# Optimization experiments

Measured on AMD Instinct MI355X. Metric: run time of the kernel, lower is better.

## Reference

```python
import jax, jax.numpy as jnp
import numpy as np

B, N, K = 4, 32768, 16
IN_DIM, HID, OUT_DIM = 32, 64, 32
N_DIM = 2
KIN = 2 * N_DIM + OUT_DIM  # 36
KH = 64
EPS = 1e-5


def _gelu(x):
    return jax.nn.gelu(x, approximate=False)  # torch F.gelu default (erf)


def setup_inputs() -> dict:
    key = jax.random.key(0)
    ks = jax.random.split(key, 16)
    s = lambda fan_in: 1.0 / np.sqrt(fan_in)
    return {
        "inp": jax.random.normal(ks[0], (B, N, IN_DIM), jnp.float32),
        "input_grid": jax.random.uniform(ks[1], (N, N_DIM), jnp.float32),
        "output_grid": jax.random.uniform(ks[2], (N, N_DIM), jnp.float32),
        "neighbor_idx": jax.random.randint(ks[3], (N, K), 0, N, jnp.int32),
        # pointwise projection MLP: in_dim -> hid -> out_dim, GELU between
        "Wp1": jax.random.normal(ks[4], (IN_DIM, HID), jnp.float32) * s(IN_DIM),
        "bp1": jnp.zeros((HID,), jnp.float32),
        "Wp2": jax.random.normal(ks[5], (HID, OUT_DIM), jnp.float32) * s(HID),
        "bp2": jnp.zeros((OUT_DIM,), jnp.float32),
        # per-edge kernel MLP: [2*n_dim+out_dim, 64, 64, out_dim], GELU between
        "Wk1": jax.random.normal(ks[6], (KIN, KH), jnp.float32) * s(KIN),
        "bk1": jnp.zeros((KH,), jnp.float32),
        "Wk2": jax.random.normal(ks[7], (KH, KH), jnp.float32) * s(KH),
        "bk2": jnp.zeros((KH,), jnp.float32),
        "Wk3": jax.random.normal(ks[8], (KH, OUT_DIM), jnp.float32) * s(KH),
        "bk3": jnp.zeros((OUT_DIM,), jnp.float32),
        # LayerNorm
        "ln_gamma": jnp.ones((OUT_DIM,), jnp.float32),
        "ln_beta": jnp.zeros((OUT_DIM,), jnp.float32),
    }


def reference(inp, input_grid, output_grid, neighbor_idx,
              Wp1, bp1, Wp2, bp2, Wk1, bk1, Wk2, bk2, Wk3, bk3,
              ln_gamma, ln_beta):
    # pointwise projection MLP
    x = _gelu(jnp.einsum('bnc,ch->bnh', inp, Wp1) + bp1)
    x = jnp.einsum('bnh,ho->bno', x, Wp2) + bp2  # (B, N, OUT_DIM)

    # neighbor gather (fixed K neighbors per output point)
    f_y = x[:, neighbor_idx, :]                      # (B, N, K, C)
    y_pos = input_grid[neighbor_idx]                 # (N, K, n_dim)
    x_pos = jnp.broadcast_to(output_grid[:, None, :], (N, K, N_DIM))
    pos_feat = jnp.concatenate([y_pos, x_pos], axis=-1)          # (N, K, 2*n_dim)
    agg = jnp.concatenate(
        [jnp.broadcast_to(pos_feat[None], (x.shape[0], N, K, 2 * N_DIM)), f_y],
        axis=-1)                                      # (B, N, K, KIN)

    # nonlinear kernel MLP k(x, y, f(y))
    h = _gelu(jnp.einsum('bnkc,ch->bnkh', agg, Wk1) + bk1)
    h = _gelu(jnp.einsum('bnkh,hg->bnkg', h, Wk2) + bk2)
    k_out = jnp.einsum('bnkg,go->bnko', h, Wk3) + bk3  # (B, N, K, OUT_DIM)

    # mean-aggregate over neighbors (integral transform)
    out = jnp.mean(k_out, axis=2)                      # (B, N, OUT_DIM)

    # residual (shapes match) + LayerNorm over channels
    out = out + x
    mu = jnp.mean(out, axis=-1, keepdims=True)
    var = jnp.mean((out - mu) ** 2, axis=-1, keepdims=True)
    out = (out - mu) * jax.lax.rsqrt(var + EPS) * ln_gamma + ln_beta
    return out
```

## Files before the change

### kernel.cpp

```cpp
#include <hip/hip_runtime.h>

#define BB 4
#define NN 32768
#define KKN 16
#define IN_DIM 32
#define HID 64
#define OUT_DIM 32
#define KH 64
#define WS 88
#define TOT (BB * NN)
#define NWAVES 4096

typedef _Float16 f16;
typedef f16 f16x2 __attribute__((ext_vector_type(2)));
typedef f16 f16x4 __attribute__((ext_vector_type(4)));
typedef f16 f16x8 __attribute__((ext_vector_type(8)));
typedef float f32x4 __attribute__((ext_vector_type(4)));
typedef __fp16 hf16x2 __attribute__((ext_vector_type(2)));
typedef unsigned int u32x4 __attribute__((ext_vector_type(4)));

#define H2(c) ((f16x2){(f16)(c), (f16)(c)})
#define U2(c) (__builtin_bit_cast(unsigned, H2(c)))

__device__ __forceinline__ unsigned cvt2u(float a, float b) {
    hf16x2 r = __builtin_amdgcn_cvt_pkrtz(a, b);
    return __builtin_bit_cast(unsigned, r);
}
__device__ __forceinline__ f16x2 cvt2(float a, float b) {
    hf16x2 r = __builtin_amdgcn_cvt_pkrtz(a, b);
    return __builtin_bit_cast(f16x2, r);
}

__device__ __forceinline__ unsigned pk_fma(unsigned a, unsigned b, unsigned c) {
    unsigned d;
    asm("v_pk_fma_f16 %0, %1, %2, %3" : "=v"(d) : "v"(a), "v"(b), "v"(c));
    return d;
}
__device__ __forceinline__ unsigned pk_mul(unsigned a, unsigned b) {
    unsigned d;
    asm("v_pk_mul_f16 %0, %1, %2" : "=v"(d) : "v"(a), "v"(b));
    return d;
}
__device__ __forceinline__ unsigned pk_add(unsigned a, unsigned b) {
    unsigned d;
    asm("v_pk_add_f16 %0, %1, %2" : "=v"(d) : "v"(a), "v"(b));
    return d;
}
__device__ __forceinline__ unsigned pk_max(unsigned a, unsigned b) {
    unsigned d;
    asm("v_pk_max_f16 %0, %1, %2" : "=v"(d) : "v"(a), "v"(b));
    return d;
}
__device__ __forceinline__ unsigned pk_min(unsigned a, unsigned b) {
    unsigned d;
    asm("v_pk_min_f16 %0, %1, %2" : "=v"(d) : "v"(a), "v"(b));
    return d;
}

struct GeluK {
    unsigned n35, p35, q4, c5, c4, c3, c2, c1, c0, half;
};
__device__ __forceinline__ GeluK gelu_consts() {
    GeluK k;
    k.n35  = U2(-3.5f);        k.p35 = U2(3.5f);
    k.q4   = U2(0.25f);        k.half = U2(0.5f);
    k.c5   = U2(-1.0110344f);  k.c4 = U2(2.85016064f);
    k.c3   = U2(-3.40439040f); k.c2 = U2(2.32402432f);
    k.c1   = U2(-1.04974080f); k.c0 = U2(0.39879504f);
    return k;
}

__device__ __forceinline__ unsigned gelu2u(unsigned x, const GeluK& k) {
    unsigned s  = pk_min(pk_max(x, k.n35), k.p35);
    unsigned s4 = pk_mul(s, k.q4);
    unsigned t  = pk_mul(s4, s4);
    unsigned g  = pk_fma(k.c5, t, k.c4);
    g = pk_fma(g, t, k.c3);
    g = pk_fma(g, t, k.c2);
    g = pk_fma(g, t, k.c1);
    g = pk_fma(g, t, k.c0);
    unsigned h  = pk_fma(s, g, k.half);
    return pk_mul(x, h);
}
__device__ __forceinline__ unsigned gelu2bu(float a, float b, unsigned bias, const GeluK& k) {
    return gelu2u(pk_add(cvt2u(a, b), bias), k);
}
__device__ __forceinline__ unsigned gelu2nu(float a, float b, const GeluK& k) {
    return gelu2u(cvt2u(a, b), k);
}

template <int CTRL>
__device__ __forceinline__ float dppadd(float v) {
    union { float f; int i; } u, r;
    u.f = v;
    r.i = __builtin_amdgcn_update_dpp(0, u.i, CTRL, 0xf, 0xf, true);
    return v + r.f;
}
__device__ __forceinline__ float rowsum16(float v) {
    v = dppadd<0xB1>(v);
    v = dppadd<0x4E>(v);
    v = dppadd<0x124>(v);
    v = dppadd<0x128>(v);
    return v;
}

__global__ __launch_bounds__(256) void point_mlp_kernel(
    const float* __restrict__ inp, const float* __restrict__ Wp1,
    const float* __restrict__ bp1, const float* __restrict__ Wp2,
    const float* __restrict__ bp2, f16* __restrict__ xhf)
{
    __shared__ __align__(16) f16 hb[4][16 * WS];
    const int tid = threadIdx.x, w = tid >> 6, lane = tid & 63;
    const int q = lane >> 4, nl = lane & 15;
    const GeluK gk = gelu_consts();

    f16x8 w1f[4];
    #pragma unroll
    for (int nb = 0; nb < 4; nb++)
        #pragma unroll
        for (int j = 0; j < 8; j++)
            w1f[nb][j] = (f16)Wp1[(q * 8 + j) * HID + nb * 16 + nl];
    f16x8 w2f[2][2];
    #pragma unroll
    for (int nb = 0; nb < 2; nb++)
        #pragma unroll
        for (int c = 0; c < 2; c++)
            #pragma unroll
            for (int j = 0; j < 8; j++) {
                int k = c * 32 + q * 8 + j, kp = ((k & 3) << 4) | (k >> 2);
                w2f[nb][c][j] = (f16)Wp2[kp * OUT_DIM + nb * 16 + nl];
            }
    const unsigned b1q0 = cvt2u(bp1[nl],      bp1[16 + nl]);
    const unsigned b1q1 = cvt2u(bp1[32 + nl], bp1[48 + nl]);
    float b2v[2];
    b2v[0] = bp2[nl]; b2v[1] = bp2[16 + nl];
    const f32x4 zq = (f32x4){0.f, 0.f, 0.f, 0.f};

    const int gw = blockIdx.x * 4 + w;
    const int nw = gridDim.x * 4;

    for (int t = gw; t < TOT / 16; t += nw) {
        const int R = t * 16;
        const float* ap = inp + (size_t)(R + nl) * IN_DIM + q * 8;
        float4 av0 = *(const float4*)ap, av1 = *(const float4*)(ap + 4);
        f16x2 p01 = cvt2(av0.x, av0.y);
        f16x2 p23 = cvt2(av0.z, av0.w);
        f16x2 p45 = cvt2(av1.x, av1.y);
        f16x2 p67 = cvt2(av1.z, av1.w);
        f16x8 af = (f16x8){p01.x, p01.y, p23.x, p23.y, p45.x, p45.y, p67.x, p67.y};

        f32x4 acc[4];
        #pragma unroll
        for (int nb = 0; nb < 4; nb++)
            acc[nb] = __builtin_amdgcn_mfma_f32_16x16x32_f16(af, w1f[nb], zq, 0, 0, 0);

        #pragma unroll
        for (int r = 0; r < 4; r++) {
            unsigned h01 = gelu2bu(acc[0][r], acc[1][r], b1q0, gk);
            unsigned h23 = gelu2bu(acc[2][r], acc[3][r], b1q1, gk);
            *(uint2*)&hb[w][(q * 4 + r) * WS + nl * 4] = (uint2){h01, h23};
        }
        f16x8 a0 = *(const f16x8*)&hb[w][nl * WS + q * 8];
        f16x8 a1 = *(const f16x8*)&hb[w][nl * WS + 32 + q * 8];
        f32x4 a2[2];
        #pragma unroll
        for (int nb = 0; nb < 2; nb++) {
            a2[nb] = (f32x4){b2v[nb], b2v[nb], b2v[nb], b2v[nb]};
            a2[nb] = __builtin_amdgcn_mfma_f32_16x16x32_f16(a0, w2f[nb][0], a2[nb], 0, 0, 0);
            a2[nb] = __builtin_amdgcn_mfma_f32_16x16x32_f16(a1, w2f[nb][1], a2[nb], 0, 0, 0);
        }
        #pragma unroll
        for (int r = 0; r < 4; r++)
            #pragma unroll
            for (int nb = 0; nb < 2; nb++)
                xhf[(size_t)(R + q * 4 + r) * OUT_DIM + nb * 16 + nl] = (f16)a2[nb][r];
    }
}

__global__ __launch_bounds__(256) void gnn_edge_kernel(
    const f16*   __restrict__ xhf,
    const float* __restrict__ igrid, const float* __restrict__ ogrid,
    const int*   __restrict__ nbi,
    const float* __restrict__ Wk1, const float* __restrict__ bk1,
    const float* __restrict__ Wk2, const float* __restrict__ bk2,
    const float* __restrict__ Wk3, const float* __restrict__ bk3,
    const float* __restrict__ gma, const float* __restrict__ bta,
    float* __restrict__ out)
{
    __shared__ __align__(16) f16 tile[8][16 * WS];

    const int tid = threadIdx.x, w = tid >> 6, lane = tid & 63;
    const int q = lane >> 4, nl = lane & 15;
    f16* __restrict__ TA = tile[w * 2];
    f16* __restrict__ TB = tile[w * 2 + 1];
    const GeluK gk = gelu_consts();

    f16x8 w1f[4][2], w2f[4][2], w3f[2][2];
    #pragma unroll
    for (int nb = 0; nb < 4; nb++) {
        #pragma unroll
        for (int j = 0; j < 8; j++) {
            w1f[nb][0][j] = (f16)Wk1[(4 + q * 8 + j) * KH + nb * 16 + nl];
            float v1 = 0.0f;
            if (j < 4 && q == 0) v1 = Wk1[j * KH + nb * 16 + nl];
            w1f[nb][1][j] = (f16)v1;
        }
        #pragma unroll
        for (int c = 0; c < 2; c++)
            #pragma unroll
            for (int j = 0; j < 8; j++) {
                int k = c * 32 + q * 8 + j, kp = ((k & 3) << 4) | (k >> 2);
                w2f[nb][c][j] = (f16)Wk2[kp * KH + nb * 16 + nl];
            }
    }
    #pragma unroll
    for (int nb = 0; nb < 2; nb++)
        #pragma unroll
        for (int c = 0; c < 2; c++)
            #pragma unroll
            for (int j = 0; j < 8; j++) {
                int k = c * 32 + q * 8 + j, kp = ((k & 3) << 4) | (k >> 2);
                w3f[nb][c][j] = (f16)(Wk3[kp * OUT_DIM + nb * 16 + nl] * 0.0625f);
            }

    const unsigned b1q0 = cvt2u(bk1[nl],      bk1[16 + nl]);
    const unsigned b1q1 = cvt2u(bk1[32 + nl], bk1[48 + nl]);
    const unsigned b2q0 = cvt2u(bk2[nl],      bk2[16 + nl]);
    const unsigned b2q1 = cvt2u(bk2[32 + nl], bk2[48 + nl]);
    float b3v[2];
    b3v[0] = bk3[nl]; b3v[1] = bk3[16 + nl];
    const float g0 = gma[nl], g1 = gma[16 + nl], be0 = bta[nl], be1 = bta[16 + nl];

    const f32x4 zq = (f32x4){0.f, 0.f, 0.f, 0.f};

    const int gw = blockIdx.x * 4 + w;

    int tA = gw, tB = gw + NWAVES;
    int nA = nbi[(tA & (NN - 1)) * KKN + nl];
    int nB = nbi[(tB & (NN - 1)) * KKN + nl];
    uint4 fyA = ((const uint4*)(xhf + ((size_t)((tA >> 15) * NN + nA)) * OUT_DIM))[q];
    uint4 fyB = ((const uint4*)(xhf + ((size_t)((tB >> 15) * NN + nB)) * OUT_DIM))[q];
    uint2 paA, paB;
    if (q == 0) {
        float2 ip, op;
        ip = ((const float2*)igrid)[nA]; op = ((const float2*)ogrid)[tA & (NN - 1)];
        paA.x = cvt2u(ip.x, ip.y); paA.y = cvt2u(op.x, op.y);
        ip = ((const float2*)igrid)[nB]; op = ((const float2*)ogrid)[tB & (NN - 1)];
        paB.x = cvt2u(ip.x, ip.y); paB.y = cvt2u(op.x, op.y);
    }
    f16 xA0 = xhf[(size_t)tA * OUT_DIM + nl],      xA1 = xhf[(size_t)tA * OUT_DIM + 16 + nl];
    f16 xB0 = xhf[(size_t)tB * OUT_DIM + nl],      xB1 = xhf[(size_t)tB * OUT_DIM + 16 + nl];

    #pragma unroll 1
    for (int it = 0; it < TOT / (2 * NWAVES); ++it) {
        const float rA0 = (float)xA0, rA1 = (float)xA1, rB0 = (float)xB0, rB1 = (float)xB1;

        const int tA2 = (tA + 2 * NWAVES) & (TOT - 1);
        const int tB2 = tA2 + NWAVES;
        const int nA2 = nbi[(tA2 & (NN - 1)) * KKN + nl];
        const int nB2 = nbi[(tB2 & (NN - 1)) * KKN + nl];

        f16x8 aA0 = __builtin_bit_cast(f16x8, fyA);
        f16x8 aB0 = __builtin_bit_cast(f16x8, fyB);
        u32x4 uA1 = (u32x4){q == 0 ? paA.x : 0u, q == 0 ? paA.y : 0u, 0u, 0u};
        u32x4 uB1 = (u32x4){q == 0 ? paB.x : 0u, q == 0 ? paB.y : 0u, 0u, 0u};
        f16x8 aA1 = __builtin_bit_cast(f16x8, uA1);
        f16x8 aB1 = __builtin_bit_cast(f16x8, uB1);

        f32x4 cA[4], cB[4];
        #pragma unroll
        for (int nb = 0; nb < 4; nb++) {
            cA[nb] = __builtin_amdgcn_mfma_f32_16x16x32_f16(aA0, w1f[nb][0], zq, 0, 0, 0);
            cB[nb] = __builtin_amdgcn_mfma_f32_16x16x32_f16(aB0, w1f[nb][0], zq, 0, 0, 0);
            cA[nb] = __builtin_amdgcn_mfma_f32_16x16x32_f16(aA1, w1f[nb][1], cA[nb], 0, 0, 0);
            cB[nb] = __builtin_amdgcn_mfma_f32_16x16x32_f16(aB1, w1f[nb][1], cB[nb], 0, 0, 0);
        }
        #pragma unroll
        for (int r = 0; r < 4; r++) {
            unsigned hA01 = gelu2bu(cA[0][r], cA[1][r], b1q0, gk);
            unsigned hA23 = gelu2bu(cA[2][r], cA[3][r], b1q1, gk);
            unsigned hB01 = gelu2bu(cB[0][r], cB[1][r], b1q0, gk);
            unsigned hB23 = gelu2bu(cB[2][r], cB[3][r], b1q1, gk);
            *(uint2*)&TA[(q * 4 + r) * WS + nl * 4] = (uint2){hA01, hA23};
            *(uint2*)&TB[(q * 4 + r) * WS + nl * 4] = (uint2){hB01, hB23};
        }

        uint4 fyA2 = ((const uint4*)(xhf + ((size_t)((tA2 >> 15) * NN + nA2)) * OUT_DIM))[q];
        uint4 fyB2 = ((const uint4*)(xhf + ((size_t)((tB2 >> 15) * NN + nB2)) * OUT_DIM))[q];
        uint2 paA2, paB2;
        if (q == 0) {
            float2 ip, op;
            ip = ((const float2*)igrid)[nA2]; op = ((const float2*)ogrid)[tA2 & (NN - 1)];
            paA2.x = cvt2u(ip.x, ip.y); paA2.y = cvt2u(op.x, op.y);
            ip = ((const float2*)igrid)[nB2]; op = ((const float2*)ogrid)[tB2 & (NN - 1)];
            paB2.x = cvt2u(ip.x, ip.y); paB2.y = cvt2u(op.x, op.y);
        }
        f16 xA0n = xhf[(size_t)tA2 * OUT_DIM + nl],  xA1n = xhf[(size_t)tA2 * OUT_DIM + 16 + nl];
        f16 xB0n = xhf[(size_t)tB2 * OUT_DIM + nl],  xB1n = xhf[(size_t)tB2 * OUT_DIM + 16 + nl];

        f16x8 bA0 = *(const f16x8*)&TA[nl * WS + q * 8];
        f16x8 bA1 = *(const f16x8*)&TA[nl * WS + 32 + q * 8];
        f16x8 bB0 = *(const f16x8*)&TB[nl * WS + q * 8];
        f16x8 bB1 = *(const f16x8*)&TB[nl * WS + 32 + q * 8];
        #pragma unroll
        for (int nb = 0; nb < 4; nb++) {
            cA[nb] = __builtin_amdgcn_mfma_f32_16x16x32_f16(bA0, w2f[nb][0], zq, 0, 0, 0);
            cB[nb] = __builtin_amdgcn_mfma_f32_16x16x32_f16(bB0, w2f[nb][0], zq, 0, 0, 0);
            cA[nb] = __builtin_amdgcn_mfma_f32_16x16x32_f16(bA1, w2f[nb][1], cA[nb], 0, 0, 0);
            cB[nb] = __builtin_amdgcn_mfma_f32_16x16x32_f16(bB1, w2f[nb][1], cB[nb], 0, 0, 0);
        }
        #pragma unroll
        for (int r = 0; r < 4; r++) {
            unsigned hA01 = gelu2bu(cA[0][r], cA[1][r], b2q0, gk);
            unsigned hA23 = gelu2bu(cA[2][r], cA[3][r], b2q1, gk);
            unsigned hB01 = gelu2bu(cB[0][r], cB[1][r], b2q0, gk);
            unsigned hB23 = gelu2bu(cB[2][r], cB[3][r], b2q1, gk);
            *(uint2*)&TA[(q * 4 + r) * WS + nl * 4] = (uint2){hA01, hA23};
            *(uint2*)&TB[(q * 4 + r) * WS + nl * 4] = (uint2){hB01, hB23};
        }

        bA0 = *(const f16x8*)&TA[nl * WS + q * 8];
        bA1 = *(const f16x8*)&TA[nl * WS + 32 + q * 8];
        bB0 = *(const f16x8*)&TB[nl * WS + q * 8];
        bB1 = *(const f16x8*)&TB[nl * WS + 32 + q * 8];
        f32x4 dA[2], dB[2];
        #pragma unroll
        for (int nb = 0; nb < 2; nb++) {
            dA[nb] = __builtin_amdgcn_mfma_f32_16x16x32_f16(bA0, w3f[nb][0], zq, 0, 0, 0);
            dB[nb] = __builtin_amdgcn_mfma_f32_16x16x32_f16(bB0, w3f[nb][0], zq, 0, 0, 0);
            dA[nb] = __builtin_amdgcn_mfma_f32_16x16x32_f16(bA1, w3f[nb][1], dA[nb], 0, 0, 0);
            dB[nb] = __builtin_amdgcn_mfma_f32_16x16x32_f16(bB1, w3f[nb][1], dB[nb], 0, 0, 0);
        }

        {
            float s0 = dA[0][0] + dA[0][1] + dA[0][2] + dA[0][3];
            float s1 = dA[1][0] + dA[1][1] + dA[1][2] + dA[1][3];
            float u0 = dB[0][0] + dB[0][1] + dB[0][2] + dB[0][3];
            float u1 = dB[1][0] + dB[1][1] + dB[1][2] + dB[1][3];
            s0 += __shfl_xor(s0, 16, 64); s0 += __shfl_xor(s0, 32, 64);
            s1 += __shfl_xor(s1, 16, 64); s1 += __shfl_xor(s1, 32, 64);
            u0 += __shfl_xor(u0, 16, 64); u0 += __shfl_xor(u0, 32, 64);
            u1 += __shfl_xor(u1, 16, 64); u1 += __shfl_xor(u1, 32, 64);

            float oA0 = s0 + b3v[0] + rA0;
            float oA1 = s1 + b3v[1] + rA1;
            float oB0 = u0 + b3v[0] + rB0;
            float oB1 = u1 + b3v[1] + rB1;

            float mA = rowsum16(oA0 + oA1) * (1.0f / 32.0f);
            float mB = rowsum16(oB0 + oB1) * (1.0f / 32.0f);
            float dA0 = oA0 - mA, dA1 = oA1 - mA, dB0 = oB0 - mB, dB1 = oB1 - mB;
            float vA = rowsum16(dA0 * dA0 + dA1 * dA1) * (1.0f / 32.0f);
            float vB = rowsum16(dB0 * dB0 + dB1 * dB1) * (1.0f / 32.0f);
            float rsA = rsqrtf(vA + 1e-5f);
            float rsB = rsqrtf(vB + 1e-5f);

            if (q == 0) {
                float* oa = out + (size_t)tA * OUT_DIM;
                float* ob = out + (size_t)tB * OUT_DIM;
                oa[nl]      = fmaf(dA0 * rsA, g0, be0);
                oa[16 + nl] = fmaf(dA1 * rsA, g1, be1);
                ob[nl]      = fmaf(dB0 * rsB, g0, be0);
                ob[16 + nl] = fmaf(dB1 * rsB, g1, be1);
            }
        }

        tA = tA2; tB = tB2;
        fyA = fyA2; fyB = fyB2;
        paA = paA2; paB = paB2;
        xA0 = xA0n; xA1 = xA1n; xB0 = xB0n; xB1 = xB1n;
    }
}

extern "C" void kernel_launch(void* const* d_in, const int* in_sizes, int n_in,
                              void* d_out, int out_size, void* d_ws, size_t ws_size,
                              hipStream_t stream) {
    const float* inp   = (const float*)d_in[0];
    const float* igrid = (const float*)d_in[1];
    const float* ogrid = (const float*)d_in[2];
    const int*   nbi   = (const int*)d_in[3];
    const float* Wp1   = (const float*)d_in[4];
    const float* bp1   = (const float*)d_in[5];
    const float* Wp2   = (const float*)d_in[6];
    const float* bp2   = (const float*)d_in[7];
    const float* Wk1   = (const float*)d_in[8];
    const float* bk1   = (const float*)d_in[9];
    const float* Wk2   = (const float*)d_in[10];
    const float* bk2   = (const float*)d_in[11];
    const float* Wk3   = (const float*)d_in[12];
    const float* bk3   = (const float*)d_in[13];
    const float* gma   = (const float*)d_in[14];
    const float* bta   = (const float*)d_in[15];
    float* out = (float*)d_out;
    f16* xhf = (f16*)d_ws;

    point_mlp_kernel<<<512, 256, 0, stream>>>(inp, Wp1, bp1, Wp2, bp2, xhf);
    gnn_edge_kernel<<<1024, 256, 0, stream>>>(xhf, igrid, ogrid, nbi,
                                              Wk1, bk1, Wk2, bk2, Wk3, bk3,
                                              gma, bta, out);
}
```

Baseline: 214.9 us.

## Stage edge-MLP weight fragments in LDS instead of registers, retune padding and grid

After: 210.2 us. -2.2%, faster.

```diff
diff --git a/kernel.cpp b/kernel.cpp
--- a/kernel.cpp
+++ b/kernel.cpp
@@ -7,7 +7,7 @@
 #define HID 64
 #define OUT_DIM 32
 #define KH 64
-#define WS 88
+#define WS 72
 #define TOT (BB * NN)
 #define NWAVES 4096
 
@@ -85,9 +85,6 @@
 __device__ __forceinline__ unsigned gelu2bu(float a, float b, unsigned bias, const GeluK& k) {
     return gelu2u(pk_add(cvt2u(a, b), bias), k);
 }
-__device__ __forceinline__ unsigned gelu2nu(float a, float b, const GeluK& k) {
-    return gelu2u(cvt2u(a, b), k);
-}
 
 template <int CTRL>
 __device__ __forceinline__ float dppadd(float v) {
@@ -188,6 +185,7 @@
     float* __restrict__ out)
 {
     __shared__ __align__(16) f16 tile[8][16 * WS];
+    __shared__ __align__(16) f16 wf[20][64][8];
 
     const int tid = threadIdx.x, w = tid >> 6, lane = tid & 63;
     const int q = lane >> 4, nl = lane & 15;
@@ -195,33 +193,41 @@
     f16* __restrict__ TB = tile[w * 2 + 1];
     const GeluK gk = gelu_consts();
 
-    f16x8 w1f[4][2], w2f[4][2], w3f[2][2];
-    #pragma unroll
-    for (int nb = 0; nb < 4; nb++) {
-        #pragma unroll
-        for (int j = 0; j < 8; j++) {
-            w1f[nb][0][j] = (f16)Wk1[(4 + q * 8 + j) * KH + nb * 16 + nl];
-            float v1 = 0.0f;
-            if (j < 4 && q == 0) v1 = Wk1[j * KH + nb * 16 + nl];
-            w1f[nb][1][j] = (f16)v1;
-        }
-        #pragma unroll
-        for (int c = 0; c < 2; c++)
+    #pragma unroll 1
+    for (int f = w * 5; f < w * 5 + 5; ++f) {
+        f16x8 v;
+        if (f < 4) {
+            int nb = f;
+            #pragma unroll
+            for (int j = 0; j < 8; j++)
+                v[j] = (f16)Wk1[(4 + q * 8 + j) * KH + nb * 16 + nl];
+        } else if (f < 8) {
+            int nb = f - 4;
+            #pragma unroll
+            for (int j = 0; j < 8; j++) {
+                float x = 0.0f;
+                if (j < 4 && q == 0) x = Wk1[j * KH + nb * 16 + nl];
+                v[j] = (f16)x;
+            }
+        } else if (f < 16) {
+            int nb = (f - 8) & 3, c = (f - 8) >> 2;
             #pragma unroll
             for (int j = 0; j < 8; j++) {
                 int k = c * 32 + q * 8 + j, kp = ((k & 3) << 4) | (k >> 2);
-                w2f[nb][c][j] = (f16)Wk2[kp * KH + nb * 16 + nl];
+                v[j] = (f16)Wk2[kp * KH + nb * 16 + nl];
             }
-    }
-    #pragma unroll
-    for (int nb = 0; nb < 2; nb++)
-        #pragma unroll
-        for (int c = 0; c < 2; c++)
+        } else {
+            int nb = (f - 16) & 1, c = (f - 16) >> 1;
             #pragma unroll
             for (int j = 0; j < 8; j++) {
                 int k = c * 32 + q * 8 + j, kp = ((k & 3) << 4) | (k >> 2);
-                w3f[nb][c][j] = (f16)(Wk3[kp * OUT_DIM + nb * 16 + nl] * 0.0625f);
+                v[j] = (f16)(Wk3[kp * OUT_DIM + nb * 16 + nl] * 0.0625f);
             }
+        }
+        *(f16x8*)&wf[f][lane][0] = v;
+    }
+    __syncthreads();
+    #define WFRAG(f) (*(const f16x8*)&wf[(f)][lane][0])
 
     const unsigned b1q0 = cvt2u(bk1[nl],      bk1[16 + nl]);
     const unsigned b1q1 = cvt2u(bk1[32 + nl], bk1[48 + nl]);
@@ -270,10 +276,15 @@
         f32x4 cA[4], cB[4];
         #pragma unroll
         for (int nb = 0; nb < 4; nb++) {
-            cA[nb] = __builtin_amdgcn_mfma_f32_16x16x32_f16(aA0, w1f[nb][0], zq, 0, 0, 0);
-            cB[nb] = __builtin_amdgcn_mfma_f32_16x16x32_f16(aB0, w1f[nb][0], zq, 0, 0, 0);
-            cA[nb] = __builtin_amdgcn_mfma_f32_16x16x32_f16(aA1, w1f[nb][1], cA[nb], 0, 0, 0);
-            cB[nb] = __builtin_amdgcn_mfma_f32_16x16x32_f16(aB1, w1f[nb][1], cB[nb], 0, 0, 0);
+            f16x8 W0 = WFRAG(nb);
+            cA[nb] = __builtin_amdgcn_mfma_f32_16x16x32_f16(aA0, W0, zq, 0, 0, 0);
+            cB[nb] = __builtin_amdgcn_mfma_f32_16x16x32_f16(aB0, W0, zq, 0, 0, 0);
+        }
+        #pragma unroll
+        for (int nb = 0; nb < 4; nb++) {
+            f16x8 W1 = WFRAG(4 + nb);
+            cA[nb] = __builtin_amdgcn_mfma_f32_16x16x32_f16(aA1, W1, cA[nb], 0, 0, 0);
+            cB[nb] = __builtin_amdgcn_mfma_f32_16x16x32_f16(aB1, W1, cB[nb], 0, 0, 0);
         }
         #pragma unroll
         for (int r = 0; r < 4; r++) {
@@ -304,10 +315,15 @@
         f16x8 bB1 = *(const f16x8*)&TB[nl * WS + 32 + q * 8];
         #pragma unroll
         for (int nb = 0; nb < 4; nb++) {
-            cA[nb] = __builtin_amdgcn_mfma_f32_16x16x32_f16(bA0, w2f[nb][0], zq, 0, 0, 0);
-            cB[nb] = __builtin_amdgcn_mfma_f32_16x16x32_f16(bB0, w2f[nb][0], zq, 0, 0, 0);
-            cA[nb] = __builtin_amdgcn_mfma_f32_16x16x32_f16(bA1, w2f[nb][1], cA[nb], 0, 0, 0);
-            cB[nb] = __builtin_amdgcn_mfma_f32_16x16x32_f16(bB1, w2f[nb][1], cB[nb], 0, 0, 0);
+            f16x8 W0 = WFRAG(8 + nb);
+            cA[nb] = __builtin_amdgcn_mfma_f32_16x16x32_f16(bA0, W0, zq, 0, 0, 0);
+            cB[nb] = __builtin_amdgcn_mfma_f32_16x16x32_f16(bB0, W0, zq, 0, 0, 0);
+        }
+        #pragma unroll
+        for (int nb = 0; nb < 4; nb++) {
+            f16x8 W1 = WFRAG(12 + nb);
+            cA[nb] = __builtin_amdgcn_mfma_f32_16x16x32_f16(bA1, W1, cA[nb], 0, 0, 0);
+            cB[nb] = __builtin_amdgcn_mfma_f32_16x16x32_f16(bB1, W1, cB[nb], 0, 0, 0);
         }
         #pragma unroll
         for (int r = 0; r < 4; r++) {
@@ -326,10 +342,15 @@
         f32x4 dA[2], dB[2];
         #pragma unroll
         for (int nb = 0; nb < 2; nb++) {
-            dA[nb] = __builtin_amdgcn_mfma_f32_16x16x32_f16(bA0, w3f[nb][0], zq, 0, 0, 0);
-            dB[nb] = __builtin_amdgcn_mfma_f32_16x16x32_f16(bB0, w3f[nb][0], zq, 0, 0, 0);
-            dA[nb] = __builtin_amdgcn_mfma_f32_16x16x32_f16(bA1, w3f[nb][1], dA[nb], 0, 0, 0);
-            dB[nb] = __builtin_amdgcn_mfma_f32_16x16x32_f16(bB1, w3f[nb][1], dB[nb], 0, 0, 0);
+            f16x8 W0 = WFRAG(16 + nb);
+            dA[nb] = __builtin_amdgcn_mfma_f32_16x16x32_f16(bA0, W0, zq, 0, 0, 0);
+            dB[nb] = __builtin_amdgcn_mfma_f32_16x16x32_f16(bB0, W0, zq, 0, 0, 0);
+        }
+        #pragma unroll
+        for (int nb = 0; nb < 2; nb++) {
+            f16x8 W1 = WFRAG(18 + nb);
+            dA[nb] = __builtin_amdgcn_mfma_f32_16x16x32_f16(bA1, W1, dA[nb], 0, 0, 0);
+            dB[nb] = __builtin_amdgcn_mfma_f32_16x16x32_f16(bB1, W1, dB[nb], 0, 0, 0);
         }
 
         {
@@ -370,6 +391,7 @@
         paA = paA2; paB = paB2;
         xA0 = xA0n; xA1 = xA1n; xB0 = xB0n; xB1 = xB1n;
     }
+    #undef WFRAG
 }
 
 extern "C" void kernel_launch(void* const* d_in, const int* in_sizes, int n_in,
@@ -394,7 +416,7 @@
     float* out = (float*)d_out;
     f16* xhf = (f16*)d_ws;
 
-    point_mlp_kernel<<<512, 256, 0, stream>>>(inp, Wp1, bp1, Wp2, bp2, xhf);
+    point_mlp_kernel<<<1024, 256, 0, stream>>>(inp, Wp1, bp1, Wp2, bp2, xhf);
     gnn_edge_kernel<<<1024, 256, 0, stream>>>(xhf, igrid, ogrid, nbi,
                                               Wk1, bk1, Wk2, bk2, Wk3, bk3,
                                               gma, bta, out);
```
